# Performance work log

Measured on AMD Instinct MI355X. Metric: run time of the kernel, lower is better.

The kernel has to match this reference:

```python
import jax, jax.numpy as jnp
import numpy as np

N_NODES = 50000
N_EDGES = 800000
X_DIM, H_DIM, Y_DIM = 128, 256, 128


def spmm(adj_vals, adj_row, adj_col, x):
    # sparse [N,N] @ dense [N,D] via gather + segment scatter-add
    msgs = adj_vals[:, None] * x[adj_col]  # [E, D]
    return jax.ops.segment_sum(msgs, adj_row, num_segments=N_NODES)


def setup_inputs() -> dict:
    key = jax.random.key(0)
    ks = jax.random.split(key, 6)
    x = jax.random.uniform(ks[0], (N_NODES, X_DIM), dtype=jnp.float32)
    adj_vals = jax.random.uniform(ks[1], (N_EDGES,), dtype=jnp.float32)
    adj_row = jax.random.randint(ks[2], (N_EDGES,), 0, N_NODES, dtype=jnp.int32)
    adj_col = jax.random.randint(ks[3], (N_EDGES,), 0, N_NODES, dtype=jnp.int32)
    W1 = jax.random.normal(ks[4], (X_DIM, H_DIM), dtype=jnp.float32) * (1.0 / np.sqrt(X_DIM))
    b1 = jnp.zeros((H_DIM,), dtype=jnp.float32)
    W2 = jax.random.normal(ks[5], (H_DIM, Y_DIM), dtype=jnp.float32) * (1.0 / np.sqrt(H_DIM))
    b2 = jnp.zeros((Y_DIM,), dtype=jnp.float32)
    return {"x": x, "adj_vals": adj_vals, "adj_row": adj_row, "adj_col": adj_col,
            "W1": W1, "b1": b1, "W2": W2, "b2": b2}


def reference(x, adj_vals, adj_row, adj_col, W1, b1, W2, b2):
    # row-normalize features: x / (sum_j x_ij + 1e-4)
    x = x / (jnp.sum(x, axis=1, keepdims=True) + 1e-4)
    # layer 1: spmm -> linear -> relu (dropout is identity at eval)
    h = jax.nn.relu(spmm(adj_vals, adj_row, adj_col, x) @ W1 + b1)  # [N, H]
    # layer 2: spmm -> linear
    y = spmm(adj_vals, adj_row, adj_col, h) @ W2 + b2  # [N, Y]
    return y
```

## Files before the change

kernel.cpp:

```cpp
#include <hip/hip_runtime.h>

#define N_NODES 50000
#define N_EDGES 800000
#define X_DIM 128
#define H_DIM 256
#define Y_DIM 128

typedef unsigned int uint32;
typedef unsigned short ushort16;
typedef __attribute__((ext_vector_type(8))) short short8;
typedef __attribute__((ext_vector_type(4))) float floatx4;

__device__ inline ushort16 f2bf(float f) {
    uint32 u = __float_as_uint(f);
    return (ushort16)((u + 0x7FFFu + ((u >> 16) & 1u)) >> 16);
}
__device__ inline float bf_lo(uint32 u) { return __uint_as_float(u << 16); }
__device__ inline float bf_hi(uint32 u) { return __uint_as_float(u & 0xFFFF0000u); }

#define BUCKET_SHIFT 7
#define NB 391
#define CHUNK 4096
#define NCHUNK 196
#define CAP_B 2560

#define NORM_BLOCKS 12500
#define CONV_BLOCKS 256

__global__ __launch_bounds__(256) void prep_kernel(
    const float* __restrict__ x, uint32* __restrict__ xb,
    const float* __restrict__ W1, const float* __restrict__ W2,
    ushort16* __restrict__ W1t, ushort16* __restrict__ W2t,
    const int* __restrict__ rows, int* __restrict__ gpartial) {
    int b = blockIdx.x;
    if (b < NORM_BLOCKS) {
        int row = (b * 256 + threadIdx.x) >> 6;
        int lane = threadIdx.x & 63;
        float2 v = ((const float2*)x)[(size_t)row * 64 + lane];
        float s = v.x + v.y;
        #pragma unroll
        for (int off = 32; off > 0; off >>= 1) s += __shfl_xor(s, off, 64);
        float inv = 1.0f / (s + 1e-4f);
        uint32 lo = (uint32)f2bf(v.x * inv);
        uint32 hi = (uint32)f2bf(v.y * inv);
        xb[(size_t)row * 64 + lane] = lo | (hi << 16);
    } else if (b < NORM_BLOCKS + CONV_BLOCKS) {
        int t = (b - NORM_BLOCKS) * 256 + threadIdx.x;
        if (t < X_DIM * H_DIM) {
            int n = t >> 7, k = t & 127;
            W1t[t] = f2bf(W1[k * H_DIM + n]);
        } else {
            int u = t - X_DIM * H_DIM;
            int y = u >> 8, k = u & 255;
            W2t[u] = f2bf(W2[k * Y_DIM + y]);
        }
    } else {
        __shared__ int h[NB];
        int j = b - NORM_BLOCKS - CONV_BLOCKS;
        int t = threadIdx.x;
        for (int i = t; i < NB; i += 256) h[i] = 0;
        __syncthreads();
        int base = j * CHUNK;
        #pragma unroll
        for (int k = 0; k < CHUNK / 256; k++) {
            int e = base + t + k * 256;
            if (e < N_EDGES) atomicAdd(&h[rows[e] >> BUCKET_SHIFT], 1);
        }
        __syncthreads();
        for (int i = t; i < NB; i += 256) gpartial[j * NB + i] = h[i];
    }
}

__global__ __launch_bounds__(512) void bucket_scan_kernel(
    const int* __restrict__ gpartial, int* __restrict__ bucket_base,
    int* __restrict__ bcursor, int* __restrict__ rowptr) {
    __shared__ int s[512];
    int t = threadIdx.x;
    int total = 0;
    if (t < NB) {
        #pragma unroll 4
        for (int j = 0; j < NCHUNK; j++) total += gpartial[j * NB + t];
    }
    s[t] = total;
    __syncthreads();
    #pragma unroll
    for (int off = 1; off < 512; off <<= 1) {
        int u = (t >= off) ? s[t - off] : 0;
        __syncthreads();
        s[t] += u;
        __syncthreads();
    }
    if (t < NB) {
        int excl = s[t] - total;
        bucket_base[t] = excl;
        bcursor[t] = excl;
    }
    if (t == 0) { bucket_base[NB] = N_EDGES; rowptr[N_NODES] = N_EDGES; }
}

__global__ __launch_bounds__(512) void bucketize_kernel(
    const int* __restrict__ rows, const int* __restrict__ cols,
    const float* __restrict__ vals, const int* __restrict__ gpartial,
    int* __restrict__ bcursor, int2* __restrict__ edges) {
    __shared__ int ob[512];
    __shared__ int c[NB];
    __shared__ int g[NB];
    __shared__ int2 buf[CHUNK];
    int t = threadIdx.x;
    int j = blockIdx.x;
    int base = j * CHUNK;
    int M = N_EDGES - base; if (M > CHUNK) M = CHUNK;
    int cnt = (t < NB) ? gpartial[j * NB + t] : 0;
    ob[t] = cnt;
    __syncthreads();
    #pragma unroll
    for (int off = 1; off < 512; off <<= 1) {
        int u = (t >= off) ? ob[t - off] : 0;
        __syncthreads();
        ob[t] += u;
        __syncthreads();
    }
    ob[t] -= cnt;
    if (t < NB) {
        c[t] = 0;
        g[t] = (cnt > 0) ? atomicAdd(&bcursor[t], cnt) : 0;
    }
    __syncthreads();
    #pragma unroll
    for (int k = 0; k < CHUNK / 512; k++) {
        int e = base + t + k * 512;
        if (e < N_EDGES) {
            int r = rows[e];
            int bb = r >> BUCKET_SHIFT;
            int p = ob[bb] + atomicAdd(&c[bb], 1);
            buf[p] = make_int2(cols[e] | ((r & 127) << 16) | (bb << 23),
                               __float_as_int(vals[e]));
        }
    }
    __syncthreads();
    for (int i = t; i < M; i += 512) {
        int2 e = buf[i];
        int bb = (int)((uint32)e.x >> 23);
        edges[g[bb] + (i - ob[bb])] = e;
    }
}

__global__ __launch_bounds__(256) void bucket_sort_kernel(
    const int* __restrict__ bucket_base, int2* __restrict__ edges,
    int2* __restrict__ scratch, int* __restrict__ rowptr) {
    __shared__ int2 buf[CAP_B];
    __shared__ int2 buf2[CAP_B];
    __shared__ int h[128], o[128], c[128];
    int b = blockIdx.x, t = threadIdx.x;
    int base = bucket_base[b];
    int cnt = bucket_base[b + 1] - base;
    bool fits = (cnt <= CAP_B);
    if (t < 128) h[t] = 0;
    __syncthreads();
    for (int i = t; i < cnt; i += 256) {
        int2 e = edges[base + i];
        if (fits) buf[i] = e; else scratch[base + i] = e;
        atomicAdd(&h[(e.x >> 16) & 127], 1);
    }
    __syncthreads();
    int valh = (t < 128) ? h[t] : 0;
    #pragma unroll
    for (int off = 1; off < 128; off <<= 1) {
        int u = (t >= off && t < 128) ? h[t - off] : 0;
        __syncthreads();
        if (t < 128) h[t] += u;
        __syncthreads();
    }
    if (t < 128) {
        o[t] = h[t] - valh;
        c[t] = 0;
        int i = (b << BUCKET_SHIFT) + t;
        if (i < N_NODES) rowptr[i] = base + h[t] - valh;
    }
    __syncthreads();
    for (int i = t; i < cnt; i += 256) {
        int2 e = fits ? buf[i] : scratch[base + i];
        int lr = (e.x >> 16) & 127;
        int p = o[lr] + atomicAdd(&c[lr], 1);
        if (fits) buf2[p] = e; else edges[base + p] = e;
    }
    __syncthreads();
    if (fits)
        for (int i = t; i < cnt; i += 256) edges[base + i] = buf2[i];
}

__device__ __forceinline__ void spmm_row2(const uint2* __restrict__ feat2,
                                          const int2* __restrict__ edges,
                                          int start, int end, int lane,
                                          float& A0, float& A1, float& A2, float& A3) {
    const int hl = lane & 31;
    const int bsrc = lane & 32;
    float x0 = 0.f, x1 = 0.f, x2 = 0.f, x3 = 0.f;
    int cur = start;
    while (__any(cur < end)) {
        int n = end - cur;
        n = n < 0 ? 0 : (n > 32 ? 32 : n);
        int2 ev = make_int2(0, 0);
        if (hl < n) ev = edges[cur + hl];
        int c = ev.x & 0xFFFF;
        float v = __int_as_float(ev.y);
        int na = __shfl(n, 0, 64), nb = __shfl(n, 32, 64);
        int nm = na > nb ? na : nb;
        int jm = (nm + 15) & ~15;
        for (int j = 0; j < jm; j += 16) {
            uint2 f[16];
            float vv[16];
            #pragma unroll
            for (int u = 0; u < 16; u++) {
                int cc = __shfl(c, bsrc + j + u, 64);
                vv[u] = __shfl(v, bsrc + j + u, 64);
                f[u] = feat2[(size_t)cc * 32 + hl];
            }
            #pragma unroll
            for (int u = 0; u < 16; u++) {
                x0 += vv[u] * bf_lo(f[u].x); x1 += vv[u] * bf_hi(f[u].x);
                x2 += vv[u] * bf_lo(f[u].y); x3 += vv[u] * bf_hi(f[u].y);
            }
        }
        cur += n;
    }
    A0 = x0; A1 = x1; A2 = x2; A3 = x3;
}

__global__ __launch_bounds__(512, 4) void spmm_gemm_fused(
    const uint32* __restrict__ xb, const int* __restrict__ rowptr,
    const int2* __restrict__ edges, const ushort16* __restrict__ W1t,
    const ushort16* __restrict__ W2t, const float* __restrict__ b1,
    ushort16* __restrict__ hw) {
    __shared__ ushort16 a_s[64 * 136];
    __shared__ ushort16 h_s[64 * 264];
    const int tx = threadIdx.x;
    const int wave = tx >> 6, lane = tx & 63;
    const int quad = lane >> 4, l16 = lane & 15;
    const int half = lane >> 5, hl = lane & 31;
    const int row0 = blockIdx.x * 64;
    const uint2* xb2 = (const uint2*)xb;

    for (int i = 0; i < 4; i++) {
        int r = wave * 8 + i * 2 + half;
        int row = row0 + r;
        int s = 0, e = 0;
        if (row < N_NODES) { s = rowptr[row]; e = rowptr[row + 1]; }
        float a0, a1, a2, a3;
        spmm_row2(xb2, edges, s, e, lane, a0, a1, a2, a3);
        uint32 lo = (uint32)f2bf(a0) | ((uint32)f2bf(a1) << 16);
        uint32 hi = (uint32)f2bf(a2) | ((uint32)f2bf(a3) << 16);
        *(uint2*)&a_s[r * 136 + hl * 4] = make_uint2(lo, hi);
    }

    short8 bfr1[2][4];
    #pragma unroll
    for (int ct = 0; ct < 2; ct++)
        #pragma unroll
        for (int kk = 0; kk < 4; kk++)
            bfr1[ct][kk] = *(const short8*)
                &W1t[(wave * 32 + ct * 16 + l16) * 128 + kk * 32 + quad * 8];
    __syncthreads();

    floatx4 acc1[4][2];
    #pragma unroll
    for (int rs = 0; rs < 4; rs++)
        #pragma unroll
        for (int ct = 0; ct < 2; ct++)
            #pragma unroll
            for (int j = 0; j < 4; j++) acc1[rs][ct][j] = 0.f;
    #pragma unroll
    for (int kk = 0; kk < 4; kk++) {
        #pragma unroll
        for (int rs = 0; rs < 4; rs++) {
            short8 af = *(const short8*)&a_s[(rs * 16 + l16) * 136 + kk * 32 + quad * 8];
            #pragma unroll
            for (int ct = 0; ct < 2; ct++)
                acc1[rs][ct] = __builtin_amdgcn_mfma_f32_16x16x32_bf16(
                    af, bfr1[ct][kk], acc1[rs][ct], 0, 0, 0);
        }
    }
    float bv[2];
    #pragma unroll
    for (int ct = 0; ct < 2; ct++) bv[ct] = b1[wave * 32 + ct * 16 + l16];
    #pragma unroll
    for (int rs = 0; rs < 4; rs++)
        #pragma unroll
        for (int ct = 0; ct < 2; ct++)
            #pragma unroll
            for (int reg = 0; reg < 4; reg++) {
                float v = acc1[rs][ct][reg] + bv[ct];
                v = v > 0.f ? v : 0.f;
                h_s[(rs * 16 + quad * 4 + reg) * 264 + wave * 32 + ct * 16 + l16] = f2bf(v);
            }

    short8 bfr2[8];
    #pragma unroll
    for (int kk = 0; kk < 8; kk++)
        bfr2[kk] = *(const short8*)
            &W2t[(wave * 16 + l16) * 256 + kk * 32 + quad * 8];
    __syncthreads();

    floatx4 acc2[4];
    #pragma unroll
    for (int rs = 0; rs < 4; rs++)
        #pragma unroll
        for (int j = 0; j < 4; j++) acc2[rs][j] = 0.f;
    #pragma unroll
    for (int kk = 0; kk < 8; kk++) {
        #pragma unroll
        for (int rs = 0; rs < 4; rs++) {
            short8 af = *(const short8*)&h_s[(rs * 16 + l16) * 264 + kk * 32 + quad * 8];
            acc2[rs] = __builtin_amdgcn_mfma_f32_16x16x32_bf16(
                af, bfr2[kk], acc2[rs], 0, 0, 0);
        }
    }
    #pragma unroll
    for (int rs = 0; rs < 4; rs++)
        #pragma unroll
        for (int reg = 0; reg < 4; reg++) {
            int row = row0 + rs * 16 + quad * 4 + reg;
            if (row < N_NODES)
                hw[(size_t)row * 128 + wave * 16 + l16] = f2bf(acc2[rs][reg]);
        }
}

__global__ __launch_bounds__(256) void spmm_out_kernel(
    const uint32* __restrict__ feat, const int* __restrict__ rowptr,
    const int2* __restrict__ edges, const float* __restrict__ bias,
    float* __restrict__ out) {
    int w = (blockIdx.x * blockDim.x + threadIdx.x) >> 6;
    int lane = threadIdx.x & 63;
    int half = lane >> 5, hl = lane & 31;
    int row = w * 2 + half;
    int s = rowptr[row], e = rowptr[row + 1];
    float a0, a1, a2, a3;
    spmm_row2((const uint2*)feat, edges, s, e, lane, a0, a1, a2, a3);
    float4 b = ((const float4*)bias)[hl];
    ((float4*)out)[(size_t)row * 32 + hl] =
        make_float4(a0 + b.x, a1 + b.y, a2 + b.z, a3 + b.w);
}

extern "C" void kernel_launch(void* const* d_in, const int* in_sizes, int n_in,
                              void* d_out, int out_size, void* d_ws, size_t ws_size,
                              hipStream_t stream) {
    const float* x = (const float*)d_in[0];
    const float* adj_vals = (const float*)d_in[1];
    const int* adj_row = (const int*)d_in[2];
    const int* adj_col = (const int*)d_in[3];
    const float* W1 = (const float*)d_in[4];
    const float* b1 = (const float*)d_in[5];
    const float* W2 = (const float*)d_in[6];
    const float* b2 = (const float*)d_in[7];
    float* out = (float*)d_out;

    char* ws = (char*)d_ws;
    uint32*   xb       = (uint32*)  (ws + 0);
    ushort16* hw       = (ushort16*)(ws + 12800000);
    int2*     edges    = (int2*)    (ws + 25600000);
    int2*     scratch  = (int2*)    (ws + 32000000);
    int*      gpartial = (int*)     (ws + 38400000);
    int*      rowptr   = (int*)     (ws + 38713344);
    int*      bbase    = (int*)     (ws + 38914048);
    int*      bcursor  = (int*)     (ws + 38916096);
    ushort16* W1t      = (ushort16*)(ws + 38918144);
    ushort16* W2t      = (ushort16*)(ws + 38983680);

    hipLaunchKernelGGL(prep_kernel, dim3(NORM_BLOCKS + CONV_BLOCKS + NCHUNK),
                       dim3(256), 0, stream, x, xb, W1, W2, W1t, W2t,
                       adj_row, gpartial);

    hipLaunchKernelGGL(bucket_scan_kernel, dim3(1), dim3(512),
                       0, stream, gpartial, bbase, bcursor, rowptr);

    hipLaunchKernelGGL(bucketize_kernel, dim3(NCHUNK), dim3(512),
                       0, stream, adj_row, adj_col, adj_vals, gpartial, bcursor, edges);
    hipLaunchKernelGGL(bucket_sort_kernel, dim3(NB), dim3(256),
                       0, stream, bbase, edges, scratch, rowptr);

    hipLaunchKernelGGL(spmm_gemm_fused, dim3((N_NODES + 63) / 64), dim3(512),
                       0, stream, xb, rowptr, edges, W1t, W2t, b1, hw);

    hipLaunchKernelGGL(spmm_out_kernel, dim3(N_NODES / 8), dim3(256),
                       0, stream, (const uint32*)hw, rowptr, edges, b2, out);
}
```

Baseline: 224.0 us.

## Fold bucket scan into bucketize and stage block edges in LDS for SpMM

```diff
diff --git a/kernel.cpp b/kernel.cpp
--- a/kernel.cpp
+++ b/kernel.cpp
@@ -23,6 +23,7 @@
 #define CHUNK 4096
 #define NCHUNK 196
 #define CAP_B 2560
+#define CAP_E 4224
 
 #define NORM_BLOCKS 12500
 #define CONV_BLOCKS 256
@@ -71,68 +72,64 @@
     }
 }
 
-__global__ __launch_bounds__(512) void bucket_scan_kernel(
-    const int* __restrict__ gpartial, int* __restrict__ bucket_base,
-    int* __restrict__ bcursor, int* __restrict__ rowptr) {
-    __shared__ int s[512];
-    int t = threadIdx.x;
-    int total = 0;
-    if (t < NB) {
-        #pragma unroll 4
-        for (int j = 0; j < NCHUNK; j++) total += gpartial[j * NB + t];
-    }
-    s[t] = total;
-    __syncthreads();
-    #pragma unroll
-    for (int off = 1; off < 512; off <<= 1) {
-        int u = (t >= off) ? s[t - off] : 0;
-        __syncthreads();
-        s[t] += u;
-        __syncthreads();
-    }
-    if (t < NB) {
-        int excl = s[t] - total;
-        bucket_base[t] = excl;
-        bcursor[t] = excl;
-    }
-    if (t == 0) { bucket_base[NB] = N_EDGES; rowptr[N_NODES] = N_EDGES; }
-}
-
 __global__ __launch_bounds__(512) void bucketize_kernel(
     const int* __restrict__ rows, const int* __restrict__ cols,
     const float* __restrict__ vals, const int* __restrict__ gpartial,
-    int* __restrict__ bcursor, int2* __restrict__ edges) {
+    int2* __restrict__ edges, int* __restrict__ bucket_base,
+    int* __restrict__ rowptr) {
+    __shared__ int sc[512];
     __shared__ int ob[512];
-    __shared__ int c[NB];
-    __shared__ int g[NB];
+    __shared__ int gw[NB];
+    __shared__ int cur[NB];
     __shared__ int2 buf[CHUNK];
     int t = threadIdx.x;
     int j = blockIdx.x;
     int base = j * CHUNK;
     int M = N_EDGES - base; if (M > CHUNK) M = CHUNK;
-    int cnt = (t < NB) ? gpartial[j * NB + t] : 0;
-    ob[t] = cnt;
+
+    int total = 0, pre = 0, cnt = 0;
+    if (t < NB) {
+        for (int jj = 0; jj < NCHUNK; jj++) {
+            int v = gpartial[jj * NB + t];
+            total += v;
+            pre += (jj < j) ? v : 0;
+        }
+        cnt = gpartial[j * NB + t];
+    }
+    sc[t] = total;
     __syncthreads();
     #pragma unroll
     for (int off = 1; off < 512; off <<= 1) {
-        int u = (t >= off) ? ob[t - off] : 0;
-        __syncthreads();
-        ob[t] += u;
-        __syncthreads();
-    }
-    ob[t] -= cnt;
-    if (t < NB) {
-        c[t] = 0;
-        g[t] = (cnt > 0) ? atomicAdd(&bcursor[t], cnt) : 0;
-    }
-    __syncthreads();
+        int u = (t >= off) ? sc[t - off] : 0;
+        __syncthreads();
+        sc[t] += u;
+        __syncthreads();
+    }
+    int bexcl = sc[t] - total;
+    if (t < NB) { gw[t] = bexcl + pre; cur[t] = 0; }
+    if (j == 0) {
+        if (t < NB) bucket_base[t] = bexcl;
+        if (t == 0) { bucket_base[NB] = N_EDGES; rowptr[N_NODES] = N_EDGES; }
+    }
+    sc[t] = cnt;
+    __syncthreads();
+    #pragma unroll
+    for (int off = 1; off < 512; off <<= 1) {
+        int u = (t >= off) ? sc[t - off] : 0;
+        __syncthreads();
+        sc[t] += u;
+        __syncthreads();
+    }
+    ob[t] = sc[t] - cnt;
+    __syncthreads();
+
     #pragma unroll
     for (int k = 0; k < CHUNK / 512; k++) {
         int e = base + t + k * 512;
         if (e < N_EDGES) {
             int r = rows[e];
             int bb = r >> BUCKET_SHIFT;
-            int p = ob[bb] + atomicAdd(&c[bb], 1);
+            int p = ob[bb] + atomicAdd(&cur[bb], 1);
             buf[p] = make_int2(cols[e] | ((r & 127) << 16) | (bb << 23),
                                __float_as_int(vals[e]));
         }
@@ -141,7 +138,7 @@
     for (int i = t; i < M; i += 512) {
         int2 e = buf[i];
         int bb = (int)((uint32)e.x >> 23);
-        edges[g[bb] + (i - ob[bb])] = e;
+        edges[gw[bb] + (i - ob[bb])] = e;
     }
 }
 
@@ -189,42 +186,62 @@
         for (int i = t; i < cnt; i += 256) edges[base + i] = buf2[i];
 }
 
-__device__ __forceinline__ void spmm_row2(const uint2* __restrict__ feat2,
-                                          const int2* __restrict__ edges,
-                                          int start, int end, int lane,
-                                          float& A0, float& A1, float& A2, float& A3) {
-    const int hl = lane & 31;
-    const int bsrc = lane & 32;
-    float x0 = 0.f, x1 = 0.f, x2 = 0.f, x3 = 0.f;
-    int cur = start;
-    while (__any(cur < end)) {
-        int n = end - cur;
-        n = n < 0 ? 0 : (n > 32 ? 32 : n);
-        int2 ev = make_int2(0, 0);
-        if (hl < n) ev = edges[cur + hl];
-        int c = ev.x & 0xFFFF;
-        float v = __int_as_float(ev.y);
-        int na = __shfl(n, 0, 64), nb = __shfl(n, 32, 64);
-        int nm = na > nb ? na : nb;
-        int jm = (nm + 15) & ~15;
-        for (int j = 0; j < jm; j += 16) {
+template <typename EPT>
+__device__ __forceinline__ void gather8rows(
+    const uint2* __restrict__ feat2, EPT ep, const int* __restrict__ rowptr,
+    int row0, int s0, int wave, int lane, float ac[4][4]) {
+    const int half = lane >> 5, hl = lane & 31;
+    #pragma unroll
+    for (int g = 0; g < 2; g++) {
+        int s[2], e[2];
+        #pragma unroll
+        for (int p = 0; p < 2; p++) {
+            int row = row0 + wave * 8 + (g * 2 + p) * 2 + half;
+            s[p] = 0; e[p] = 0;
+            if (row < N_NODES) {
+                s[p] = rowptr[row] - s0;
+                e[p] = rowptr[row + 1] - s0;
+            }
+        }
+        int k0 = s[0], k1 = s[1];
+        float a00 = 0.f, a01 = 0.f, a02 = 0.f, a03 = 0.f;
+        float a10 = 0.f, a11 = 0.f, a12 = 0.f, a13 = 0.f;
+        while (k0 < e[0] || k1 < e[1]) {
+            int cc[16]; float vv[16];
+            #pragma unroll
+            for (int u = 0; u < 8; u++) {
+                int idx = k0 + u; bool ok = idx < e[0]; idx = ok ? idx : s[0];
+                int2 ee = ep[idx];
+                cc[u] = ee.x & 0xFFFF;
+                vv[u] = ok ? __int_as_float(ee.y) : 0.f;
+            }
+            #pragma unroll
+            for (int u = 0; u < 8; u++) {
+                int idx = k1 + u; bool ok = idx < e[1]; idx = ok ? idx : s[1];
+                int2 ee = ep[idx];
+                cc[8 + u] = ee.x & 0xFFFF;
+                vv[8 + u] = ok ? __int_as_float(ee.y) : 0.f;
+            }
             uint2 f[16];
-            float vv[16];
-            #pragma unroll
-            for (int u = 0; u < 16; u++) {
-                int cc = __shfl(c, bsrc + j + u, 64);
-                vv[u] = __shfl(v, bsrc + j + u, 64);
-                f[u] = feat2[(size_t)cc * 32 + hl];
-            }
-            #pragma unroll
-            for (int u = 0; u < 16; u++) {
-                x0 += vv[u] * bf_lo(f[u].x); x1 += vv[u] * bf_hi(f[u].x);
-                x2 += vv[u] * bf_lo(f[u].y); x3 += vv[u] * bf_hi(f[u].y);
-            }
-        }
-        cur += n;
-    }
-    A0 = x0; A1 = x1; A2 = x2; A3 = x3;
+            #pragma unroll
+            for (int u = 0; u < 16; u++) f[u] = feat2[(size_t)cc[u] * 32 + hl];
+            #pragma unroll
+            for (int u = 0; u < 8; u++) {
+                a00 += vv[u] * bf_lo(f[u].x); a01 += vv[u] * bf_hi(f[u].x);
+                a02 += vv[u] * bf_lo(f[u].y); a03 += vv[u] * bf_hi(f[u].y);
+            }
+            #pragma unroll
+            for (int u = 0; u < 8; u++) {
+                a10 += vv[8 + u] * bf_lo(f[8 + u].x); a11 += vv[8 + u] * bf_hi(f[8 + u].x);
+                a12 += vv[8 + u] * bf_lo(f[8 + u].y); a13 += vv[8 + u] * bf_hi(f[8 + u].y);
+            }
+            k0 += 8; k1 += 8;
+        }
+        ac[g * 2 + 0][0] = a00; ac[g * 2 + 0][1] = a01;
+        ac[g * 2 + 0][2] = a02; ac[g * 2 + 0][3] = a03;
+        ac[g * 2 + 1][0] = a10; ac[g * 2 + 1][1] = a11;
+        ac[g * 2 + 1][2] = a12; ac[g * 2 + 1][3] = a13;
+    }
 }
 
 __global__ __launch_bounds__(512, 4) void spmm_gemm_fused(
@@ -233,7 +250,9 @@
     const ushort16* __restrict__ W2t, const float* __restrict__ b1,
     ushort16* __restrict__ hw) {
     __shared__ ushort16 a_s[64 * 136];
-    __shared__ ushort16 h_s[64 * 264];
+    __shared__ int4 u_s[CAP_E / 2];
+    int2* esh = (int2*)u_s;
+    ushort16* h_s = (ushort16*)u_s;
     const int tx = threadIdx.x;
     const int wave = tx >> 6, lane = tx & 63;
     const int quad = lane >> 4, l16 = lane & 15;
@@ -241,15 +260,22 @@
     const int row0 = blockIdx.x * 64;
     const uint2* xb2 = (const uint2*)xb;
 
+    int rend = row0 + 64; if (rend > N_NODES) rend = N_NODES;
+    int s0 = rowptr[row0];
+    int cnt = rowptr[rend] - s0;
+    bool fits = (cnt <= CAP_E);
+    if (fits)
+        for (int i = tx; i < cnt; i += 512) esh[i] = edges[s0 + i];
+    __syncthreads();
+
+    float ac[4][4];
+    if (fits) gather8rows(xb2, (const int2*)esh, rowptr, row0, s0, wave, lane, ac);
+    else      gather8rows(xb2, edges + s0,       rowptr, row0, s0, wave, lane, ac);
+    #pragma unroll
     for (int i = 0; i < 4; i++) {
         int r = wave * 8 + i * 2 + half;
-        int row = row0 + r;
-        int s = 0, e = 0;
-        if (row < N_NODES) { s = rowptr[row]; e = rowptr[row + 1]; }
-        float a0, a1, a2, a3;
-        spmm_row2(xb2, edges, s, e, lane, a0, a1, a2, a3);
-        uint32 lo = (uint32)f2bf(a0) | ((uint32)f2bf(a1) << 16);
-        uint32 hi = (uint32)f2bf(a2) | ((uint32)f2bf(a3) << 16);
+        uint32 lo = (uint32)f2bf(ac[i][0]) | ((uint32)f2bf(ac[i][1]) << 16);
+        uint32 hi = (uint32)f2bf(ac[i][2]) | ((uint32)f2bf(ac[i][3]) << 16);
         *(uint2*)&a_s[r * 136 + hl * 4] = make_uint2(lo, hi);
     }
 
@@ -325,20 +351,38 @@
         }
 }
 
-__global__ __launch_bounds__(256) void spmm_out_kernel(
+__global__ __launch_bounds__(512, 4) void spmm_out_kernel(
     const uint32* __restrict__ feat, const int* __restrict__ rowptr,
     const int2* __restrict__ edges, const float* __restrict__ bias,
     float* __restrict__ out) {
-    int w = (blockIdx.x * blockDim.x + threadIdx.x) >> 6;
-    int lane = threadIdx.x & 63;
-    int half = lane >> 5, hl = lane & 31;
-    int row = w * 2 + half;
-    int s = rowptr[row], e = rowptr[row + 1];
-    float a0, a1, a2, a3;
-    spmm_row2((const uint2*)feat, edges, s, e, lane, a0, a1, a2, a3);
+    __shared__ int2 esh[CAP_E];
+    const int tx = threadIdx.x;
+    const int wave = tx >> 6, lane = tx & 63;
+    const int half = lane >> 5, hl = lane & 31;
+    const int row0 = blockIdx.x * 64;
+    const uint2* f2 = (const uint2*)feat;
+
+    int rend = row0 + 64; if (rend > N_NODES) rend = N_NODES;
+    int s0 = rowptr[row0];
+    int cnt = rowptr[rend] - s0;
+    bool fits = (cnt <= CAP_E);
+    if (fits)
+        for (int i = tx; i < cnt; i += 512) esh[i] = edges[s0 + i];
+    __syncthreads();
+
+    float ac[4][4];
+    if (fits) gather8rows(f2, (const int2*)esh, rowptr, row0, s0, wave, lane, ac);
+    else      gather8rows(f2, edges + s0,       rowptr, row0, s0, wave, lane, ac);
+
     float4 b = ((const float4*)bias)[hl];
-    ((float4*)out)[(size_t)row * 32 + hl] =
-        make_float4(a0 + b.x, a1 + b.y, a2 + b.z, a3 + b.w);
+    #pragma unroll
+    for (int i = 0; i < 4; i++) {
+        int row = row0 + wave * 8 + i * 2 + half;
+        if (row < N_NODES)
+            ((float4*)out)[(size_t)row * 32 + hl] =
+                make_float4(ac[i][0] + b.x, ac[i][1] + b.y,
+                            ac[i][2] + b.z, ac[i][3] + b.w);
+    }
 }
 
 extern "C" void kernel_launch(void* const* d_in, const int* in_sizes, int n_in,
@@ -362,7 +406,6 @@
     int*      gpartial = (int*)     (ws + 38400000);
     int*      rowptr   = (int*)     (ws + 38713344);
     int*      bbase    = (int*)     (ws + 38914048);
-    int*      bcursor  = (int*)     (ws + 38916096);
     ushort16* W1t      = (ushort16*)(ws + 38918144);
     ushort16* W2t      = (ushort16*)(ws + 38983680);
 
@@ -370,17 +413,16 @@
                        dim3(256), 0, stream, x, xb, W1, W2, W1t, W2t,
                        adj_row, gpartial);
 
-    hipLaunchKernelGGL(bucket_scan_kernel, dim3(1), dim3(512),
-                       0, stream, gpartial, bbase, bcursor, rowptr);
-
     hipLaunchKernelGGL(bucketize_kernel, dim3(NCHUNK), dim3(512),
-                       0, stream, adj_row, adj_col, adj_vals, gpartial, bcursor, edges);
+                       0, stream, adj_row, adj_col, adj_vals, gpartial,
+                       edges, bbase, rowptr);
+
     hipLaunchKernelGGL(bucket_sort_kernel, dim3(NB), dim3(256),
                        0, stream, bbase, edges, scratch, rowptr);
 
     hipLaunchKernelGGL(spmm_gemm_fused, dim3((N_NODES + 63) / 64), dim3(512),
                        0, stream, xb, rowptr, edges, W1t, W2t, b1, hw);
 
-    hipLaunchKernelGGL(spmm_out_kernel, dim3(N_NODES / 8), dim3(256),
+    hipLaunchKernelGGL(spmm_out_kernel, dim3((N_NODES + 63) / 64), dim3(512),
                        0, stream, (const uint32*)hw, rowptr, edges, b2, out);
 }
```

New measurement: 222.5 us. No clear change (-0.6%).
